# Kernel optimization log

Hardware: AMD Instinct MI355X
Metric: run time of the kernel (lower is better)

## Reference

```python
import jax, jax.numpy as jnp
import numpy as np

B, N, M = 256, 4096, 64
EPS = 1e-16

def setup_inputs() -> dict:
    key = jax.random.key(0)
    ks = jax.random.split(key, 9)
    memory = jax.random.normal(ks[0], (B, N, M), dtype=jnp.float32) * 0.1
    k = jax.random.normal(ks[1], (B, M), dtype=jnp.float32)
    beta = jax.random.uniform(ks[2], (B, 1), dtype=jnp.float32) * 5.0  # key strength > 0
    g = jax.random.uniform(ks[3], (B, 1), dtype=jnp.float32)           # gate in [0,1)
    s = jax.nn.softmax(jax.random.normal(ks[4], (B, 3), dtype=jnp.float32), axis=1)  # shift dist
    gamma = 1.0 + jax.random.uniform(ks[5], (B, 1), dtype=jnp.float32) * 2.0  # sharpen >= 1
    w_prev = jax.nn.softmax(jax.random.normal(ks[6], (B, N), dtype=jnp.float32), axis=1)
    e = jax.random.uniform(ks[7], (B, M), dtype=jnp.float32)  # erase in [0,1)
    a = jax.random.normal(ks[8], (B, M), dtype=jnp.float32)   # add vector
    return {"memory": memory, "k": k, "beta": beta, "g": g, "s": s,
            "gamma": gamma, "w_prev": w_prev, "e": e, "a": a}


def reference(memory, k, beta, g, s, gamma, w_prev, e, a):
    # --- address (section 3.3) ---
    # cosine similarity (torch F.cosine_similarity semantics: norms clamped at 1e-8)
    mem_e = memory + EPS                       # [B,N,M]
    k_e = (k + EPS)[:, None, :]                # [B,1,M]
    num = jnp.sum(mem_e * k_e, axis=-1)        # [B,N]
    mem_n = jnp.maximum(jnp.sqrt(jnp.sum(mem_e * mem_e, axis=-1)), 1e-8)
    k_n = jnp.maximum(jnp.sqrt(jnp.sum(k_e * k_e, axis=-1)), 1e-8)
    cos = num / (mem_n * k_n)                  # [B,N]
    wc = jax.nn.softmax(beta * cos, axis=1)    # content weighting
    # interpolate with previous weighting
    wg = g * wc + (1.0 - g) * w_prev           # [B,N]
    # circular convolution with 3-tap shift kernel s:
    # out[n] = s0*wg[n-1] + s1*wg[n] + s2*wg[n+1]  (circular)
    w_hat = (s[:, 0:1] * jnp.roll(wg, 1, axis=1)
             + s[:, 1:2] * wg
             + s[:, 2:3] * jnp.roll(wg, -1, axis=1))
    # sharpen
    wp = w_hat ** gamma
    w = wp / (jnp.sum(wp, axis=1, keepdims=True) + EPS)
    # --- read (section 3.1) ---
    rd = jnp.einsum('bn,bnm->bm', w, memory)
    # --- write (section 3.2): erase then add via outer products ---
    erase = w[:, :, None] * e[:, None, :]      # [B,N,M]
    add = w[:, :, None] * a[:, None, :]        # [B,N,M]
    new_mem = memory * (1.0 - erase) + add
    return rd, new_mem, w
```

## Files before the change

kernel.cpp:

```cpp
#include <hip/hip_runtime.h>
#include <math.h>

#define Bdim 256
#define Ndim 4096
#define Mdim 64
#define EPSF 1e-16f

typedef float vf4 __attribute__((ext_vector_type(4)));

__global__ __launch_bounds__(256) void pass_a_kernel(
    const float* __restrict__ mem, const float* __restrict__ k,
    float* __restrict__ q)
{
    const int blocks_per_b = Ndim / 64;
    const int b = blockIdx.x / blocks_per_b;
    const int rowbase = (blockIdx.x % blocks_per_b) * 64;
    const int t = threadIdx.x;
    const int m4 = t & 15;
    const int rsub = t >> 4;

    float4 ke = reinterpret_cast<const float4*>(k + b * Mdim)[m4];
    ke.x += EPSF; ke.y += EPSF; ke.z += EPSF; ke.w += EPSF;

    const float4* memb = reinterpret_cast<const float4*>(mem + (size_t)b * Ndim * Mdim);

    #pragma unroll
    for (int it = 0; it < 4; ++it) {
        const int row = rowbase + it * 16 + rsub;
        float4 mv = memb[row * 16 + m4];
        mv.x += EPSF; mv.y += EPSF; mv.z += EPSF; mv.w += EPSF;
        float d  = mv.x * ke.x + mv.y * ke.y + mv.z * ke.z + mv.w * ke.w;
        float nr = mv.x * mv.x + mv.y * mv.y + mv.z * mv.z + mv.w * mv.w;
        #pragma unroll
        for (int mask = 1; mask < 16; mask <<= 1) {
            d  += __shfl_xor(d, mask);
            nr += __shfl_xor(nr, mask);
        }
        if (m4 == 0) {
            const float mn = fmaxf(sqrtf(nr), 1e-8f);
            q[b * Ndim + row] = d / mn;
        }
    }
}

__device__ __forceinline__ float block_reduce_sum(float v, float* red, int t)
{
    const int lane = t & 63, wave = t >> 6;
    #pragma unroll
    for (int mask = 32; mask; mask >>= 1) v += __shfl_xor(v, mask);
    __syncthreads();
    if (lane == 0) red[wave] = v;
    __syncthreads();
    return red[0] + red[1] + red[2] + red[3];
}

__device__ __forceinline__ float block_reduce_max(float v, float* red, int t)
{
    const int lane = t & 63, wave = t >> 6;
    #pragma unroll
    for (int mask = 32; mask; mask >>= 1) v = fmaxf(v, __shfl_xor(v, mask));
    __syncthreads();
    if (lane == 0) red[wave] = v;
    __syncthreads();
    return fmaxf(fmaxf(red[0], red[1]), fmaxf(red[2], red[3]));
}

__global__ __launch_bounds__(256) void pass_b_kernel(
    const float* __restrict__ q, const float* __restrict__ k,
    const float* __restrict__ beta, const float* __restrict__ g,
    const float* __restrict__ s, const float* __restrict__ gamma,
    const float* __restrict__ w_prev, float* __restrict__ w_out,
    float* __restrict__ rd)
{
    __shared__ float wg_lds[Ndim];
    __shared__ float red[4];
    __shared__ float sh_kn;

    const int b = blockIdx.x;
    const int t = threadIdx.x;
    const int lane = t & 63, wave = t >> 6;

    if (wave == 1) rd[b * Mdim + lane] = 0.0f;

    if (wave == 0) {
        float v = k[b * Mdim + lane] + EPSF;
        float sq = v * v;
        #pragma unroll
        for (int mask = 32; mask; mask >>= 1) sq += __shfl_xor(sq, mask);
        if (lane == 0) sh_kn = fmaxf(sqrtf(sq), 1e-8f);
    }
    __syncthreads();

    const float beta_eff = beta[b] / sh_kn;
    const float gb = g[b];
    const float s0 = s[b * 3 + 0], s1 = s[b * 3 + 1], s2 = s[b * 3 + 2];
    const float gam = gamma[b];

    const float4* q4  = reinterpret_cast<const float4*>(q + (size_t)b * Ndim);
    const float4* wp4 = reinterpret_cast<const float4*>(w_prev + (size_t)b * Ndim);

    float4 zv[4];
    float zmax = -1e30f;
    #pragma unroll
    for (int i = 0; i < 4; ++i) {
        float4 v = q4[t + i * 256];
        v.x *= beta_eff; v.y *= beta_eff; v.z *= beta_eff; v.w *= beta_eff;
        zv[i] = v;
        zmax = fmaxf(zmax, fmaxf(fmaxf(v.x, v.y), fmaxf(v.z, v.w)));
    }
    zmax = block_reduce_max(zmax, red, t);

    float esum = 0.f;
    #pragma unroll
    for (int i = 0; i < 4; ++i) {
        zv[i].x = expf(zv[i].x - zmax); zv[i].y = expf(zv[i].y - zmax);
        zv[i].z = expf(zv[i].z - zmax); zv[i].w = expf(zv[i].w - zmax);
        esum += zv[i].x + zv[i].y + zv[i].z + zv[i].w;
    }
    esum = block_reduce_sum(esum, red, t);
    const float inv_esum = 1.0f / esum;

    float4 wgv[4];
    #pragma unroll
    for (int i = 0; i < 4; ++i) {
        float4 wp = wp4[t + i * 256];
        float4 w;
        w.x = gb * (zv[i].x * inv_esum) + (1.f - gb) * wp.x;
        w.y = gb * (zv[i].y * inv_esum) + (1.f - gb) * wp.y;
        w.z = gb * (zv[i].z * inv_esum) + (1.f - gb) * wp.z;
        w.w = gb * (zv[i].w * inv_esum) + (1.f - gb) * wp.w;
        wgv[i] = w;
        reinterpret_cast<float4*>(wg_lds)[t + i * 256] = w;
    }
    __syncthreads();

    float4 wpv[4];
    float psum = 0.f;
    #pragma unroll
    for (int i = 0; i < 4; ++i) {
        const int n0 = 4 * (t + i * 256);
        const float left  = wg_lds[(n0 + Ndim - 1) & (Ndim - 1)];
        const float right = wg_lds[(n0 + 4) & (Ndim - 1)];
        const float4 w = wgv[i];
        float4 h;
        h.x = s0 * left + s1 * w.x + s2 * w.y;
        h.y = s0 * w.x  + s1 * w.y + s2 * w.z;
        h.z = s0 * w.y  + s1 * w.z + s2 * w.w;
        h.w = s0 * w.z  + s1 * w.w + s2 * right;
        h.x = powf(h.x, gam); h.y = powf(h.y, gam);
        h.z = powf(h.z, gam); h.w = powf(h.w, gam);
        wpv[i] = h;
        psum += h.x + h.y + h.z + h.w;
    }
    psum = block_reduce_sum(psum, red, t);
    const float inv_psum = 1.0f / (psum + EPSF);

    float4* wout4 = reinterpret_cast<float4*>(w_out + (size_t)b * Ndim);
    #pragma unroll
    for (int i = 0; i < 4; ++i) {
        float4 h = wpv[i];
        h.x *= inv_psum; h.y *= inv_psum; h.z *= inv_psum; h.w *= inv_psum;
        wout4[t + i * 256] = h;
    }
}

#define NCHUNK_C 8

__global__ __launch_bounds__(256) void pass_c_kernel(
    const float* __restrict__ mem, const float* __restrict__ e,
    const float* __restrict__ a, const float* __restrict__ w,
    float* __restrict__ rd, float* __restrict__ new_mem)
{
    const int idx = (Bdim * NCHUNK_C - 1) - (int)blockIdx.x;
    const int b = idx / NCHUNK_C;
    const int chunk = idx % NCHUNK_C;
    const int rowbase = chunk * (Ndim / NCHUNK_C);
    const int t = threadIdx.x;
    const int m4 = t & 15;
    const int rsub = t >> 4;
    const int lane = t & 63, wave = t >> 6;

    float4 ev4 = reinterpret_cast<const float4*>(e + b * Mdim)[m4];
    float4 av4 = reinterpret_cast<const float4*>(a + b * Mdim)[m4];
    vf4 ev = {ev4.x, ev4.y, ev4.z, ev4.w};
    vf4 av = {av4.x, av4.y, av4.z, av4.w};

    const vf4* memb = reinterpret_cast<const vf4*>(mem + (size_t)b * Ndim * Mdim);
    vf4* nmb = reinterpret_cast<vf4*>(new_mem + (size_t)b * Ndim * Mdim);
    const float* wb = w + (size_t)b * Ndim;

    vf4 acc = {0.f, 0.f, 0.f, 0.f};

    #pragma unroll 4
    for (int it2 = 0; it2 < (Ndim / NCHUNK_C) / 16; ++it2) {
        const int it = ((Ndim / NCHUNK_C) / 16 - 1) - it2;
        const int row = rowbase + it * 16 + rsub;
        const float wr = wb[row];
        vf4 mv = memb[row * 16 + m4];
        acc += wr * mv;
        vf4 nm = mv * (1.f - wr * ev) + wr * av;
        __builtin_nontemporal_store(nm, &nmb[row * 16 + m4]);
    }

    #pragma unroll
    for (int mask = 16; mask <= 32; mask <<= 1) {
        acc.x += __shfl_xor(acc.x, mask);
        acc.y += __shfl_xor(acc.y, mask);
        acc.z += __shfl_xor(acc.z, mask);
        acc.w += __shfl_xor(acc.w, mask);
    }

    __shared__ vf4 redc[4][16];
    if (lane < 16) redc[wave][lane] = acc;
    __syncthreads();

    if (t < 16) {
        vf4 tot = redc[0][t];
        #pragma unroll
        for (int wv = 1; wv < 4; ++wv) tot += redc[wv][t];
        float* dst = rd + b * Mdim + t * 4;
        atomicAdd(dst + 0, tot.x);
        atomicAdd(dst + 1, tot.y);
        atomicAdd(dst + 2, tot.z);
        atomicAdd(dst + 3, tot.w);
    }
}

extern "C" void kernel_launch(void* const* d_in, const int* in_sizes, int n_in,
                              void* d_out, int out_size, void* d_ws, size_t ws_size,
                              hipStream_t stream)
{
    const float* mem    = (const float*)d_in[0];
    const float* k      = (const float*)d_in[1];
    const float* beta   = (const float*)d_in[2];
    const float* g      = (const float*)d_in[3];
    const float* s      = (const float*)d_in[4];
    const float* gamma  = (const float*)d_in[5];
    const float* w_prev = (const float*)d_in[6];
    const float* e      = (const float*)d_in[7];
    const float* a      = (const float*)d_in[8];

    float* out     = (float*)d_out;
    float* rd      = out;
    float* new_mem = out + Bdim * Mdim;
    float* w_out   = out + Bdim * Mdim + (size_t)Bdim * Ndim * Mdim;

    float* q = (float*)d_ws;

    pass_a_kernel<<<Bdim * (Ndim / 64), 256, 0, stream>>>(mem, k, q);
    pass_b_kernel<<<Bdim, 256, 0, stream>>>(q, k, beta, g, s, gamma, w_prev, w_out, rd);
    pass_c_kernel<<<Bdim * NCHUNK_C, 256, 0, stream>>>(mem, e, a, w_out, rd, new_mem);
}
```

Baseline: 505.4 us.

## Fuse addressing, read and write passes into one block-per-batch kernel

Merges the three kernels into a single kernel with one 1024-thread block per batch row. The cosine scores and weights stay in LDS instead of going through global workspace, and the read vector is written directly instead of accumulated with atomics. The second sweep over memory runs in reverse order to hit cache lines from the first sweep. The cost is only 256 blocks, one per CU, with barriers between phases, which may limit memory-level parallelism.

```diff
diff --git a/kernel.cpp b/kernel.cpp
--- a/kernel.cpp
+++ b/kernel.cpp
@@ -8,42 +8,7 @@
 
 typedef float vf4 __attribute__((ext_vector_type(4)));
 
-__global__ __launch_bounds__(256) void pass_a_kernel(
-    const float* __restrict__ mem, const float* __restrict__ k,
-    float* __restrict__ q)
-{
-    const int blocks_per_b = Ndim / 64;
-    const int b = blockIdx.x / blocks_per_b;
-    const int rowbase = (blockIdx.x % blocks_per_b) * 64;
-    const int t = threadIdx.x;
-    const int m4 = t & 15;
-    const int rsub = t >> 4;
-
-    float4 ke = reinterpret_cast<const float4*>(k + b * Mdim)[m4];
-    ke.x += EPSF; ke.y += EPSF; ke.z += EPSF; ke.w += EPSF;
-
-    const float4* memb = reinterpret_cast<const float4*>(mem + (size_t)b * Ndim * Mdim);
-
-    #pragma unroll
-    for (int it = 0; it < 4; ++it) {
-        const int row = rowbase + it * 16 + rsub;
-        float4 mv = memb[row * 16 + m4];
-        mv.x += EPSF; mv.y += EPSF; mv.z += EPSF; mv.w += EPSF;
-        float d  = mv.x * ke.x + mv.y * ke.y + mv.z * ke.z + mv.w * ke.w;
-        float nr = mv.x * mv.x + mv.y * mv.y + mv.z * mv.z + mv.w * mv.w;
-        #pragma unroll
-        for (int mask = 1; mask < 16; mask <<= 1) {
-            d  += __shfl_xor(d, mask);
-            nr += __shfl_xor(nr, mask);
-        }
-        if (m4 == 0) {
-            const float mn = fmaxf(sqrtf(nr), 1e-8f);
-            q[b * Ndim + row] = d / mn;
-        }
-    }
-}
-
-__device__ __forceinline__ float block_reduce_sum(float v, float* red, int t)
+__device__ __forceinline__ float block_reduce_sum16(float v, float* red, int t)
 {
     const int lane = t & 63, wave = t >> 6;
     #pragma unroll
@@ -51,10 +16,13 @@
     __syncthreads();
     if (lane == 0) red[wave] = v;
     __syncthreads();
-    return red[0] + red[1] + red[2] + red[3];
+    float sum = 0.f;
+    #pragma unroll
+    for (int i = 0; i < 16; ++i) sum += red[i];
+    return sum;
 }
 
-__device__ __forceinline__ float block_reduce_max(float v, float* red, int t)
+__device__ __forceinline__ float block_reduce_max16(float v, float* red, int t)
 {
     const int lane = t & 63, wave = t >> 6;
     #pragma unroll
@@ -62,25 +30,32 @@
     __syncthreads();
     if (lane == 0) red[wave] = v;
     __syncthreads();
-    return fmaxf(fmaxf(red[0], red[1]), fmaxf(red[2], red[3]));
+    float m = red[0];
+    #pragma unroll
+    for (int i = 1; i < 16; ++i) m = fmaxf(m, red[i]);
+    return m;
 }
 
-__global__ __launch_bounds__(256) void pass_b_kernel(
-    const float* __restrict__ q, const float* __restrict__ k,
+__global__ __launch_bounds__(1024) void ntm_fused_kernel(
+    const float* __restrict__ mem, const float* __restrict__ k,
     const float* __restrict__ beta, const float* __restrict__ g,
     const float* __restrict__ s, const float* __restrict__ gamma,
-    const float* __restrict__ w_prev, float* __restrict__ w_out,
-    float* __restrict__ rd)
+    const float* __restrict__ w_prev, const float* __restrict__ e,
+    const float* __restrict__ a,
+    float* __restrict__ rd, float* __restrict__ new_mem,
+    float* __restrict__ w_out)
 {
-    __shared__ float wg_lds[Ndim];
-    __shared__ float red[4];
+    __shared__ float q_lds[Ndim];
+    __shared__ float w_lds[Ndim];
+    __shared__ float red[16];
+    __shared__ vf4   redc[16][16];
     __shared__ float sh_kn;
 
     const int b = blockIdx.x;
     const int t = threadIdx.x;
+    const int m4 = t & 15;
+    const int rsub = t >> 4;
     const int lane = t & 63, wave = t >> 6;
-
-    if (wave == 1) rd[b * Mdim + lane] = 0.0f;
 
     if (wave == 0) {
         float v = k[b * Mdim + lane] + EPSF;
@@ -89,6 +64,26 @@
         for (int mask = 32; mask; mask >>= 1) sq += __shfl_xor(sq, mask);
         if (lane == 0) sh_kn = fmaxf(sqrtf(sq), 1e-8f);
     }
+
+    float4 ke = reinterpret_cast<const float4*>(k + b * Mdim)[m4];
+    ke.x += EPSF; ke.y += EPSF; ke.z += EPSF; ke.w += EPSF;
+
+    const vf4* memb = reinterpret_cast<const vf4*>(mem + (size_t)b * Ndim * Mdim);
+
+    #pragma unroll 4
+    for (int sweep = 0; sweep < Ndim / 64; ++sweep) {
+        const int row = sweep * 64 + rsub;
+        vf4 mv = memb[row * 16 + m4];
+        mv += EPSF;
+        float d  = mv.x * ke.x + mv.y * ke.y + mv.z * ke.z + mv.w * ke.w;
+        float nr = mv.x * mv.x + mv.y * mv.y + mv.z * mv.z + mv.w * mv.w;
+        #pragma unroll
+        for (int mask = 1; mask < 16; mask <<= 1) {
+            d  += __shfl_xor(d, mask);
+            nr += __shfl_xor(nr, mask);
+        }
+        if (m4 == 0) q_lds[row] = d / fmaxf(sqrtf(nr), 1e-8f);
+    }
     __syncthreads();
 
     const float beta_eff = beta[b] / sh_kn;
@@ -96,106 +91,56 @@
     const float s0 = s[b * 3 + 0], s1 = s[b * 3 + 1], s2 = s[b * 3 + 2];
     const float gam = gamma[b];
 
-    const float4* q4  = reinterpret_cast<const float4*>(q + (size_t)b * Ndim);
-    const float4* wp4 = reinterpret_cast<const float4*>(w_prev + (size_t)b * Ndim);
+    vf4 z = reinterpret_cast<const vf4*>(q_lds)[t] * beta_eff;
+    float zmax = fmaxf(fmaxf(z.x, z.y), fmaxf(z.z, z.w));
+    zmax = block_reduce_max16(zmax, red, t);
 
-    float4 zv[4];
-    float zmax = -1e30f;
-    #pragma unroll
-    for (int i = 0; i < 4; ++i) {
-        float4 v = q4[t + i * 256];
-        v.x *= beta_eff; v.y *= beta_eff; v.z *= beta_eff; v.w *= beta_eff;
-        zv[i] = v;
-        zmax = fmaxf(zmax, fmaxf(fmaxf(v.x, v.y), fmaxf(v.z, v.w)));
-    }
-    zmax = block_reduce_max(zmax, red, t);
-
-    float esum = 0.f;
-    #pragma unroll
-    for (int i = 0; i < 4; ++i) {
-        zv[i].x = expf(zv[i].x - zmax); zv[i].y = expf(zv[i].y - zmax);
-        zv[i].z = expf(zv[i].z - zmax); zv[i].w = expf(zv[i].w - zmax);
-        esum += zv[i].x + zv[i].y + zv[i].z + zv[i].w;
-    }
-    esum = block_reduce_sum(esum, red, t);
+    z.x = expf(z.x - zmax); z.y = expf(z.y - zmax);
+    z.z = expf(z.z - zmax); z.w = expf(z.w - zmax);
+    float esum = z.x + z.y + z.z + z.w;
+    esum = block_reduce_sum16(esum, red, t);
     const float inv_esum = 1.0f / esum;
 
-    float4 wgv[4];
-    #pragma unroll
-    for (int i = 0; i < 4; ++i) {
-        float4 wp = wp4[t + i * 256];
-        float4 w;
-        w.x = gb * (zv[i].x * inv_esum) + (1.f - gb) * wp.x;
-        w.y = gb * (zv[i].y * inv_esum) + (1.f - gb) * wp.y;
-        w.z = gb * (zv[i].z * inv_esum) + (1.f - gb) * wp.z;
-        w.w = gb * (zv[i].w * inv_esum) + (1.f - gb) * wp.w;
-        wgv[i] = w;
-        reinterpret_cast<float4*>(wg_lds)[t + i * 256] = w;
-    }
+    const float4 wp4 = reinterpret_cast<const float4*>(w_prev + (size_t)b * Ndim)[t];
+    vf4 wg;
+    wg.x = gb * (z.x * inv_esum) + (1.f - gb) * wp4.x;
+    wg.y = gb * (z.y * inv_esum) + (1.f - gb) * wp4.y;
+    wg.z = gb * (z.z * inv_esum) + (1.f - gb) * wp4.z;
+    wg.w = gb * (z.w * inv_esum) + (1.f - gb) * wp4.w;
+    reinterpret_cast<vf4*>(w_lds)[t] = wg;
     __syncthreads();
 
-    float4 wpv[4];
-    float psum = 0.f;
-    #pragma unroll
-    for (int i = 0; i < 4; ++i) {
-        const int n0 = 4 * (t + i * 256);
-        const float left  = wg_lds[(n0 + Ndim - 1) & (Ndim - 1)];
-        const float right = wg_lds[(n0 + 4) & (Ndim - 1)];
-        const float4 w = wgv[i];
-        float4 h;
-        h.x = s0 * left + s1 * w.x + s2 * w.y;
-        h.y = s0 * w.x  + s1 * w.y + s2 * w.z;
-        h.z = s0 * w.y  + s1 * w.z + s2 * w.w;
-        h.w = s0 * w.z  + s1 * w.w + s2 * right;
-        h.x = powf(h.x, gam); h.y = powf(h.y, gam);
-        h.z = powf(h.z, gam); h.w = powf(h.w, gam);
-        wpv[i] = h;
-        psum += h.x + h.y + h.z + h.w;
-    }
-    psum = block_reduce_sum(psum, red, t);
+    const int n0 = 4 * t;
+    const float left  = w_lds[(n0 + Ndim - 1) & (Ndim - 1)];
+    const float right = w_lds[(n0 + 4) & (Ndim - 1)];
+    vf4 h;
+    h.x = s0 * left + s1 * wg.x + s2 * wg.y;
+    h.y = s0 * wg.x + s1 * wg.y + s2 * wg.z;
+    h.z = s0 * wg.y + s1 * wg.z + s2 * wg.w;
+    h.w = s0 * wg.z + s1 * wg.w + s2 * right;
+    h.x = powf(h.x, gam); h.y = powf(h.y, gam);
+    h.z = powf(h.z, gam); h.w = powf(h.w, gam);
+    float psum = h.x + h.y + h.z + h.w;
+    psum = block_reduce_sum16(psum, red, t);
     const float inv_psum = 1.0f / (psum + EPSF);
+    h *= inv_psum;
 
-    float4* wout4 = reinterpret_cast<float4*>(w_out + (size_t)b * Ndim);
-    #pragma unroll
-    for (int i = 0; i < 4; ++i) {
-        float4 h = wpv[i];
-        h.x *= inv_psum; h.y *= inv_psum; h.z *= inv_psum; h.w *= inv_psum;
-        wout4[t + i * 256] = h;
-    }
-}
+    reinterpret_cast<vf4*>(w_lds)[t] = h;
+    reinterpret_cast<vf4*>(w_out + (size_t)b * Ndim)[t] = h;
+    __syncthreads();
 
-#define NCHUNK_C 8
-
-__global__ __launch_bounds__(256) void pass_c_kernel(
-    const float* __restrict__ mem, const float* __restrict__ e,
-    const float* __restrict__ a, const float* __restrict__ w,
-    float* __restrict__ rd, float* __restrict__ new_mem)
-{
-    const int idx = (Bdim * NCHUNK_C - 1) - (int)blockIdx.x;
-    const int b = idx / NCHUNK_C;
-    const int chunk = idx % NCHUNK_C;
-    const int rowbase = chunk * (Ndim / NCHUNK_C);
-    const int t = threadIdx.x;
-    const int m4 = t & 15;
-    const int rsub = t >> 4;
-    const int lane = t & 63, wave = t >> 6;
-
-    float4 ev4 = reinterpret_cast<const float4*>(e + b * Mdim)[m4];
-    float4 av4 = reinterpret_cast<const float4*>(a + b * Mdim)[m4];
-    vf4 ev = {ev4.x, ev4.y, ev4.z, ev4.w};
-    vf4 av = {av4.x, av4.y, av4.z, av4.w};
-
-    const vf4* memb = reinterpret_cast<const vf4*>(mem + (size_t)b * Ndim * Mdim);
+    const float4 ev4 = reinterpret_cast<const float4*>(e + b * Mdim)[m4];
+    const float4 av4 = reinterpret_cast<const float4*>(a + b * Mdim)[m4];
+    const vf4 ev = {ev4.x, ev4.y, ev4.z, ev4.w};
+    const vf4 av = {av4.x, av4.y, av4.z, av4.w};
     vf4* nmb = reinterpret_cast<vf4*>(new_mem + (size_t)b * Ndim * Mdim);
-    const float* wb = w + (size_t)b * Ndim;
 
     vf4 acc = {0.f, 0.f, 0.f, 0.f};
-
     #pragma unroll 4
-    for (int it2 = 0; it2 < (Ndim / NCHUNK_C) / 16; ++it2) {
-        const int it = ((Ndim / NCHUNK_C) / 16 - 1) - it2;
-        const int row = rowbase + it * 16 + rsub;
-        const float wr = wb[row];
+    for (int s2i = 0; s2i < Ndim / 64; ++s2i) {
+        const int sweep = (Ndim / 64 - 1) - s2i;
+        const int row = sweep * 64 + rsub;
+        const float wr = w_lds[row];
         vf4 mv = memb[row * 16 + m4];
         acc += wr * mv;
         vf4 nm = mv * (1.f - wr * ev) + wr * av;
@@ -209,20 +154,14 @@
         acc.z += __shfl_xor(acc.z, mask);
         acc.w += __shfl_xor(acc.w, mask);
     }
-
-    __shared__ vf4 redc[4][16];
     if (lane < 16) redc[wave][lane] = acc;
     __syncthreads();
 
     if (t < 16) {
         vf4 tot = redc[0][t];
         #pragma unroll
-        for (int wv = 1; wv < 4; ++wv) tot += redc[wv][t];
-        float* dst = rd + b * Mdim + t * 4;
-        atomicAdd(dst + 0, tot.x);
-        atomicAdd(dst + 1, tot.y);
-        atomicAdd(dst + 2, tot.z);
-        atomicAdd(dst + 3, tot.w);
+        for (int wv = 1; wv < 16; ++wv) tot += redc[wv][t];
+        reinterpret_cast<vf4*>(rd + b * Mdim)[t] = tot;
     }
 }
 
@@ -245,9 +184,6 @@
     float* new_mem = out + Bdim * Mdim;
     float* w_out   = out + Bdim * Mdim + (size_t)Bdim * Ndim * Mdim;
 
-    float* q = (float*)d_ws;
-
-    pass_a_kernel<<<Bdim * (Ndim / 64), 256, 0, stream>>>(mem, k, q);
-    pass_b_kernel<<<Bdim, 256, 0, stream>>>(q, k, beta, g, s, gamma, w_prev, w_out, rd);
-    pass_c_kernel<<<Bdim * NCHUNK_C, 256, 0, stream>>>(mem, e, a, w_out, rd, new_mem);
+    ntm_fused_kernel<<<Bdim, 1024, 0, stream>>>(
+        mem, k, beta, g, s, gamma, w_prev, e, a, rd, new_mem, w_out);
 }
```

After: 511.9 us. About the same (+1.3%).
